# Optimization experiments

Measured on AMD Instinct MI355X. Metric: run time of the kernel, lower is better.

Reference implementation:

```python
import jax, jax.numpy as jnp
import numpy as np
from jax import lax

N_IN = 200000
N_OUT = 400000
K3 = 27
M = 100000
C_IN = 128
C_OUT = 128
EPS = 1e-5


def setup_inputs() -> dict:
    key = jax.random.key(0)
    k1, k2, k3, k4 = jax.random.split(key, 4)
    feats = jax.random.normal(k1, (N_IN, C_IN), dtype=jnp.float32)
    W = jax.random.normal(k2, (K3, C_IN, C_OUT), dtype=jnp.float32) * (1.0 / np.sqrt(C_IN))
    gamma = jnp.ones((C_OUT,), dtype=jnp.float32)
    beta = jnp.zeros((C_OUT,), dtype=jnp.float32)
    in_maps = jax.random.randint(k3, (K3, M), 0, N_IN, dtype=jnp.int32)
    out_maps = jax.random.randint(k4, (K3, M), 0, N_OUT, dtype=jnp.int32)
    return {"feats": feats, "W": W, "gamma": gamma, "beta": beta,
            "in_maps": in_maps, "out_maps": out_maps, "n_out": N_OUT}


def sparse_conv_transpose(feats, W, in_maps, out_maps, n_out):
    # gather-GEMM-scatter over K3 kernel offsets (fixed small set -> scan)
    out0 = jnp.zeros((n_out, W.shape[-1]), dtype=feats.dtype)

    def body(out, xs):
        im, om, Wk = xs                      # [M], [M], [C_in, C_out]
        contrib = feats[im] @ Wk             # gather [M, C_in] -> GEMM -> [M, C_out]
        return out.at[om].add(contrib), None  # scatter-add

    out, _ = lax.scan(body, out0, (in_maps, out_maps, W))
    return out


def reference(feats, W, gamma, beta, in_maps, out_maps, n_out):
    out = sparse_conv_transpose(feats, W, in_maps, out_maps, n_out)  # [N_out, C_out]
    # MinkowskiBatchNorm (training mode): per-channel stats over all points
    mean = jnp.mean(out, axis=0)
    var = jnp.var(out, axis=0)
    y = (out - mean) * lax.rsqrt(var + EPS) * gamma + beta
    return y
```

## Files before the change

kernel.cpp:

```cpp
#include <hip/hip_runtime.h>
#include <hip/hip_fp16.h>

#define K3c    27
#define Mc     100000
#define NINc   200000
#define NOUTc  400000
#define Cc     128
#define EPSc   1e-5f

#define NBUCK  6250
#define NCNTA  (K3c * NBUCK)
#define NCNTG  NOUTc
#define BPK    391
#define SCANBA 165
#define SCANBG 391

#define WS_STATS   0u
#define WS_CNTA    4096u
#define WS_AUXA    679936u
#define WS_CNTG    681984u
#define WS_AUXG    2282496u
#define WS_WFH     2285568u
#define WS_WFL     3170304u
#define WS_SIMA    4055040u
#define WS_PGA     14855040u
#define WS_CBUF    25657344u

typedef __attribute__((ext_vector_type(8))) short short8;
typedef __attribute__((ext_vector_type(4))) float f32x4;

__device__ inline unsigned fbits(float f) { return __builtin_bit_cast(unsigned, f); }
__device__ inline float bfloat(unsigned u) { return __builtin_bit_cast(float, u); }

__device__ inline unsigned pack_hi2(float f0, float f1) {
    return (fbits(f0) >> 16) | (fbits(f1) & 0xFFFF0000u);
}
__device__ inline float trunc_bf16_f(float f) { return bfloat(fbits(f) & 0xFFFF0000u); }

__device__ inline unsigned short bf16_rne(float f) {
    unsigned u = fbits(f);
    u += 0x7FFFu + ((u >> 16) & 1u);
    return (unsigned short)(u >> 16);
}

__device__ inline unsigned short f2h(float f) { return __half_as_ushort(__float2half(f)); }
__device__ inline float h2f(unsigned short u) { return __half2float(__ushort_as_half(u)); }

__device__ inline void storeC(unsigned short* p, float v) { *p = f2h(v); }
__device__ inline void storeC(float* p, float v) { *p = v; }

__global__ __launch_bounds__(256) void zero3_kernel(float* __restrict__ stats,
                                                    unsigned* __restrict__ cntA,
                                                    unsigned* __restrict__ cntG) {
    int idx = blockIdx.x * 256 + threadIdx.x;
    if (idx < NCNTA) cntA[idx] = 0u;
    if (idx < NCNTG) cntG[idx] = 0u;
    if (idx < 512) stats[idx] = 0.f;
}

__global__ __launch_bounds__(256) void wprep_kernel(const float* __restrict__ W,
                                                    short8* __restrict__ wfh,
                                                    short8* __restrict__ wfl) {
    int tid = blockIdx.x * 256 + threadIdx.x;
    int k     = tid >> 11;
    int rem   = tid & 2047;
    int kstep = rem >> 9;
    int cb    = (rem >> 6) & 7;
    int lane  = rem & 63;
    int n   = cb * 16 + (lane & 15);
    int kk0 = kstep * 32 + (lane >> 4) * 8;
    const float* src = W + k * (Cc * Cc) + kk0 * Cc + n;
    short8 h, l;
#pragma unroll
    for (int j = 0; j < 8; ++j) {
        float f = src[j * Cc];
        unsigned short hb = bf16_rne(f);
        h[j] = (short)hb;
        float hf = bfloat(((unsigned)hb) << 16);
        l[j] = (short)bf16_rne(f - hf);
    }
    wfh[tid] = h;
    wfl[tid] = l;
}

__global__ __launch_bounds__(256) void hist3_kernel(const int* __restrict__ out_maps,
                                                    unsigned* __restrict__ cntA,
                                                    unsigned* __restrict__ cntG) {
    int b = blockIdx.x;
    int k = b / BPK;
    int m = (b - k * BPK) * 256 + threadIdx.x;
    if (m < Mc) {
        int om = out_maps[k * Mc + m];
        atomicAdd(&cntA[k * NBUCK + (om >> 6)], 1u);
        atomicAdd(&cntG[om], 1u);
    }
}

__global__ __launch_bounds__(1024) void scan_a(unsigned* __restrict__ c,
                                               unsigned* __restrict__ aux, int n) {
    __shared__ unsigned lds[1024];
    const int t = threadIdx.x;
    const int i = blockIdx.x * 1024 + t;
    unsigned v = (i < n) ? c[i] : 0u;
    lds[t] = v;
    __syncthreads();
    for (int off = 1; off < 1024; off <<= 1) {
        unsigned x = (t >= off) ? lds[t - off] : 0u;
        __syncthreads();
        lds[t] += x;
        __syncthreads();
    }
    if (i < n) c[i] = lds[t] - v;
    if (t == 1023) aux[blockIdx.x] = lds[1023];
}

__global__ __launch_bounds__(1024) void scan_b(unsigned* __restrict__ aux, int nb) {
    __shared__ unsigned lds[1024];
    const int t = threadIdx.x;
    unsigned v = (t < nb) ? aux[t] : 0u;
    lds[t] = v;
    __syncthreads();
    for (int off = 1; off < 1024; off <<= 1) {
        unsigned x = (t >= off) ? lds[t - off] : 0u;
        __syncthreads();
        lds[t] += x;
        __syncthreads();
    }
    if (t < nb) aux[t] = lds[t] - v;
}

__global__ __launch_bounds__(1024) void scan_c(unsigned* __restrict__ c,
                                               const unsigned* __restrict__ aux, int n) {
    const int i = blockIdx.x * 1024 + threadIdx.x;
    if (i < n) c[i] += aux[blockIdx.x];
}

__global__ __launch_bounds__(256) void build3_kernel(const int* __restrict__ in_maps,
                                                     const int* __restrict__ out_maps,
                                                     unsigned* __restrict__ cntA,
                                                     unsigned* __restrict__ cntG,
                                                     int* __restrict__ simA,
                                                     unsigned* __restrict__ pgA) {
    int b = blockIdx.x;
    int k = b / BPK;
    int m = (b - k * BPK) * 256 + threadIdx.x;
    if (m < Mc) {
        int om = out_maps[k * Mc + m];
        int im = in_maps[k * Mc + m];
        unsigned posA = atomicAdd(&cntA[k * NBUCK + (om >> 6)], 1u);
        unsigned posG = atomicAdd(&cntG[om], 1u);
        simA[posA] = im;
        pgA[posA]  = posG;
    }
}

template <typename ST>
__global__ __launch_bounds__(256) void phaseA_kernel(
    const float* __restrict__ feats,
    const short8* __restrict__ wfh, const short8* __restrict__ wfl,
    const unsigned* __restrict__ endA,
    const unsigned* __restrict__ endG,
    const int* __restrict__ simA, const unsigned* __restrict__ pgA,
    ST* __restrict__ cbuf, int B0, int B1, int CPSL, unsigned capRows)
{
    __shared__ short fsh[64 * 136];
    __shared__ short fsl[64 * 136];
    __shared__ unsigned posr[64];

    const int t  = threadIdx.x;
    const int bx = blockIdx.x;
    const int k  = bx / CPSL;
    const int ci = bx - k * CPSL;
    const unsigned lo = (k == 0 && B0 == 0) ? 0u : endA[k * NBUCK + B0 - 1];
    const unsigned hi = endA[k * NBUCK + B1 - 1];
    const unsigned start = lo + (unsigned)ci * 64u;
    if (start >= hi) return;
    const int valid = (int)(hi - start < 64u ? hi - start : 64u);
    const unsigned slabBase = (B0 == 0) ? 0u : endG[B0 * 64 - 1];

    {
        const int r  = t >> 2;
        const int cg = t & 3;
        const bool ok = (r < valid);
        long im = ok ? (long)simA[start + r] : 0;
        if (cg == 0) posr[r] = ok ? (pgA[start + r] - slabBase) : 0xFFFFFFFFu;
        const float4* src4 = (const float4*)(feats + im * Cc + cg * 32);
        unsigned* fh32 = (unsigned*)fsh;
        unsigned* fl32 = (unsigned*)fsl;
#pragma unroll
        for (int j = 0; j < 8; ++j) {
            float4 v = ok ? src4[j] : make_float4(0.f, 0.f, 0.f, 0.f);
            int col = cg * 32 + j * 4;
            int idx = r * 68 + (col >> 1);
            fh32[idx]     = pack_hi2(v.x, v.y);
            fh32[idx + 1] = pack_hi2(v.z, v.w);
            float lx = v.x - trunc_bf16_f(v.x);
            float ly = v.y - trunc_bf16_f(v.y);
            float lz = v.z - trunc_bf16_f(v.z);
            float lw = v.w - trunc_bf16_f(v.w);
            fl32[idx]     = pack_hi2(lx, ly);
            fl32[idx + 1] = pack_hi2(lz, lw);
        }
    }
    __syncthreads();

    const int wave = t >> 6;
    const int lane = t & 63;
    const int m    = lane & 15;
    const int quad = lane >> 4;

    f32x4 acc[8];
#pragma unroll
    for (int cb = 0; cb < 8; ++cb) acc[cb] = (f32x4){0.f, 0.f, 0.f, 0.f};

    const int arow = wave * 16 + m;
    for (int kstep = 0; kstep < 4; ++kstep) {
        const short* ah = fsh + arow * 136 + kstep * 32 + quad * 8;
        const short* al = fsl + arow * 136 + kstep * 32 + quad * 8;
        short8 a_hi = *(const short8*)ah;
        short8 a_lo = *(const short8*)al;
        int fb = ((k * 4 + kstep) * 8) * 64 + lane;
#pragma unroll
        for (int cb = 0; cb < 8; ++cb) {
            short8 b_hi = wfh[fb + cb * 64];
            short8 b_lo = wfl[fb + cb * 64];
            acc[cb] = __builtin_amdgcn_mfma_f32_16x16x32_bf16(a_hi, b_hi, acc[cb], 0, 0, 0);
            acc[cb] = __builtin_amdgcn_mfma_f32_16x16x32_bf16(a_lo, b_hi, acc[cb], 0, 0, 0);
            acc[cb] = __builtin_amdgcn_mfma_f32_16x16x32_bf16(a_hi, b_lo, acc[cb], 0, 0, 0);
        }
    }

    const int rbase = wave * 16 + quad * 4;
#pragma unroll
    for (int reg = 0; reg < 4; ++reg) {
        int row = rbase + reg;
        if (row < valid) {
            unsigned rp = posr[row];
            if (rp < capRows) {
                ST* dst = cbuf + (size_t)rp * Cc + m;
#pragma unroll
                for (int cb = 0; cb < 8; ++cb)
                    storeC(dst + cb * 16, acc[cb][reg]);
            }
        }
    }
}

template <typename ST>
__global__ __launch_bounds__(256) void phaseB_kernel(
    const ST* __restrict__ cbuf, const unsigned* __restrict__ endG,
    float* __restrict__ out, int B0)
{
    __shared__ unsigned ends[66];
    const int t = threadIdx.x;
    const int bucket = B0 + blockIdx.x;
    const int om0 = bucket * 64;
    if (t < 65) ends[t] = (om0 + t == 0) ? 0u : endG[om0 + t - 1];
    if (t == 65) ends[65] = (B0 == 0) ? 0u : endG[B0 * 64 - 1];
    __syncthreads();
    const unsigned sbase = ends[65];
    const int r  = t >> 2;
    const int cg = t & 3;
    unsigned e0 = ends[r] - sbase;
    unsigned e1 = ends[r + 1] - sbase;

    float a[32];
#pragma unroll
    for (int j = 0; j < 32; ++j) a[j] = 0.f;

    for (unsigned e = e0; e < e1; ++e) {
        const ST* src = cbuf + (size_t)e * Cc + cg * 32;
        if constexpr (sizeof(ST) == 2) {
            const short8* s8 = (const short8*)src;
#pragma unroll
            for (int p = 0; p < 4; ++p) {
                short8 v = s8[p];
#pragma unroll
                for (int j = 0; j < 8; ++j)
                    a[p * 8 + j] += h2f((unsigned short)v[j]);
            }
        } else {
            const float4* f4 = (const float4*)src;
#pragma unroll
            for (int p = 0; p < 8; ++p) {
                float4 v = f4[p];
                a[p * 4 + 0] += v.x; a[p * 4 + 1] += v.y;
                a[p * 4 + 2] += v.z; a[p * 4 + 3] += v.w;
            }
        }
    }

    float4* dst = (float4*)(out + (size_t)(om0 + r) * Cc + cg * 32);
#pragma unroll
    for (int p = 0; p < 8; ++p)
        dst[p] = make_float4(a[p * 4], a[p * 4 + 1], a[p * 4 + 2], a[p * 4 + 3]);
}

__global__ __launch_bounds__(256) void stats_kernel(const float4* __restrict__ out4,
                                                    float* __restrict__ stats) {
    const int t  = threadIdx.x;
    const int tx = t & 31;
    const int ty = t >> 5;

    float4 s = make_float4(0.f, 0.f, 0.f, 0.f);
    float4 q = make_float4(0.f, 0.f, 0.f, 0.f);
    int row0 = blockIdx.x * 400 + ty;
    for (int j = 0; j < 50; ++j) {
        float4 v = out4[(row0 + j * 8) * 32 + tx];
        s.x += v.x; s.y += v.y; s.z += v.z; s.w += v.w;
        q.x += v.x * v.x; q.y += v.y * v.y; q.z += v.z * v.z; q.w += v.w * v.w;
    }

    __shared__ float4 redS[256];
    __shared__ float4 redQ[256];
    redS[t] = s; redQ[t] = q;
    __syncthreads();
    if (ty == 0) {
#pragma unroll
        for (int jj = 1; jj < 8; ++jj) {
            float4 o = redS[jj * 32 + tx];
            s.x += o.x; s.y += o.y; s.z += o.z; s.w += o.w;
            float4 oq = redQ[jj * 32 + tx];
            q.x += oq.x; q.y += oq.y; q.z += oq.z; q.w += oq.w;
        }
        unsafeAtomicAdd(&stats[tx * 4 + 0], s.x);
        unsafeAtomicAdd(&stats[tx * 4 + 1], s.y);
        unsafeAtomicAdd(&stats[tx * 4 + 2], s.z);
        unsafeAtomicAdd(&stats[tx * 4 + 3], s.w);
        unsafeAtomicAdd(&stats[Cc + tx * 4 + 0], q.x);
        unsafeAtomicAdd(&stats[Cc + tx * 4 + 1], q.y);
        unsafeAtomicAdd(&stats[Cc + tx * 4 + 2], q.z);
        unsafeAtomicAdd(&stats[Cc + tx * 4 + 3], q.w);
    }
}

__global__ void finalize_kernel(const float* __restrict__ gamma,
                                const float* __restrict__ beta,
                                float* __restrict__ stats) {
    int c = threadIdx.x;
    float inv_n = 1.0f / (float)NOUTc;
    float mean = stats[c] * inv_n;
    float var  = stats[Cc + c] * inv_n - mean * mean;
    float scale = gamma[c] * rsqrtf(var + EPSc);
    stats[2 * Cc + c] = scale;
    stats[3 * Cc + c] = beta[c] - mean * scale;
}

__global__ __launch_bounds__(256) void norm_kernel(float4* __restrict__ out4,
                                                   const float* __restrict__ stats) {
    const float4* stats4 = (const float4*)stats;
    int idx0 = blockIdx.x * blockDim.x + threadIdx.x;
    int c4 = idx0 & 31;
    float4 sc = stats4[64 + c4];
    float4 sh = stats4[96 + c4];
    const int n4 = NOUTc * (Cc / 4);
    const int stride = gridDim.x * blockDim.x;
    for (int i = idx0; i < n4; i += stride) {
        float4 v = out4[i];
        v.x = v.x * sc.x + sh.x;
        v.y = v.y * sc.y + sh.y;
        v.z = v.z * sc.z + sh.z;
        v.w = v.w * sc.w + sh.w;
        out4[i] = v;
    }
}

extern "C" void kernel_launch(void* const* d_in, const int* in_sizes, int n_in,
                              void* d_out, int out_size, void* d_ws, size_t ws_size,
                              hipStream_t stream) {
    const float* feats    = (const float*)d_in[0];
    const float* W        = (const float*)d_in[1];
    const float* gamma    = (const float*)d_in[2];
    const float* beta     = (const float*)d_in[3];
    const int*   in_maps  = (const int*)d_in[4];
    const int*   out_maps = (const int*)d_in[5];
    float* out = (float*)d_out;

    char* ws = (char*)d_ws;
    float*    stats = (float*)(ws + WS_STATS);
    unsigned* cntA  = (unsigned*)(ws + WS_CNTA);
    unsigned* auxA  = (unsigned*)(ws + WS_AUXA);
    unsigned* cntG  = (unsigned*)(ws + WS_CNTG);
    unsigned* auxG  = (unsigned*)(ws + WS_AUXG);
    short8*   wfh   = (short8*)(ws + WS_WFH);
    short8*   wfl   = (short8*)(ws + WS_WFL);
    int*      simA  = (int*)(ws + WS_SIMA);
    unsigned* pgA   = (unsigned*)(ws + WS_PGA);

    zero3_kernel<<<1563, 256, 0, stream>>>(stats, cntA, cntG);
    wprep_kernel<<<216, 256, 0, stream>>>(W, wfh, wfl);
    hist3_kernel<<<K3c * BPK, 256, 0, stream>>>(out_maps, cntA, cntG);
    scan_a<<<SCANBA, 1024, 0, stream>>>(cntA, auxA, NCNTA);
    scan_b<<<1, 1024, 0, stream>>>(auxA, SCANBA);
    scan_c<<<SCANBA, 1024, 0, stream>>>(cntA, auxA, NCNTA);
    scan_a<<<SCANBG, 1024, 0, stream>>>(cntG, auxG, NCNTG);
    scan_b<<<1, 1024, 0, stream>>>(auxG, SCANBG);
    scan_c<<<SCANBG, 1024, 0, stream>>>(cntG, auxG, NCNTG);
    build3_kernel<<<K3c * BPK, 256, 0, stream>>>(in_maps, out_maps, cntA, cntG,
                                                 simA, pgA);

    size_t cap = (ws_size > WS_CBUF) ? (size_t)(ws_size - WS_CBUF) : 0;
    auto slabs_for = [&](size_t eb) -> int {
        for (int n = 1; n <= 64; ++n) {
            double rows = 2700000.0 / n * 1.04 + 4096.0;
            if ((size_t)rows * 128ull * eb <= cap) return n;
        }
        return -1;
    };
    int n32 = slabs_for(4);
    int n16 = slabs_for(2);
    bool use_f32 = (n32 > 0 && n32 <= 8);
    int nslab = use_f32 ? n32 : (n16 > 0 ? n16 : 64);
    const int SB = (NBUCK + nslab - 1) / nslab;
    const int CPSL = (int)(16.0 * SB * 1.10 / 64.0) + 3;

    for (int s = 0; s < nslab; ++s) {
        int B0 = s * SB;
        int B1 = (B0 + SB < NBUCK) ? B0 + SB : NBUCK;
        if (B0 >= B1) break;
        if (use_f32) {
            unsigned capRows = (unsigned)(cap / (128ull * 4ull));
            float* cbuf = (float*)(ws + WS_CBUF);
            phaseA_kernel<float><<<K3c * CPSL, 256, 0, stream>>>(
                feats, wfh, wfl, cntA, cntG, simA, pgA, cbuf, B0, B1, CPSL, capRows);
            phaseB_kernel<float><<<B1 - B0, 256, 0, stream>>>(cbuf, cntG, out, B0);
        } else {
            unsigned capRows = (unsigned)(cap / (128ull * 2ull));
            unsigned short* cbuf = (unsigned short*)(ws + WS_CBUF);
            phaseA_kernel<unsigned short><<<K3c * CPSL, 256, 0, stream>>>(
                feats, wfh, wfl, cntA, cntG, simA, pgA, cbuf, B0, B1, CPSL, capRows);
            phaseB_kernel<unsigned short><<<B1 - B0, 256, 0, stream>>>(cbuf, cntG, out, B0);
        }
    }

    stats_kernel<<<1000, 256, 0, stream>>>((const float4*)out, stats);
    finalize_kernel<<<1, 128, 0, stream>>>(gamma, beta, stats);
    norm_kernel<<<4096, 256, 0, stream>>>((float4*)out, stats);
}
```

Baseline: 2.515 ms.

## Process four 64-row chunks per phaseA block with register-resident weights and prefetch

Each phaseA block now handles up to four 64-row chunks instead of one. Each wave keeps its slice of the weight matrix (two output column blocks, hi and lo) in registers for the whole block instead of reloading it from global memory per chunk. The gather of the next chunk's feature rows is issued before the MFMA work on the current chunk, and launch bounds request 3 blocks per CU. The aim is to cut weight reloads and hide gather latency, at the cost of higher register pressure and fewer, longer blocks.

```diff
diff --git a/kernel.cpp b/kernel.cpp
--- a/kernel.cpp
+++ b/kernel.cpp
@@ -14,6 +14,7 @@
 #define BPK    391
 #define SCANBA 165
 #define SCANBG 391
+#define NCH    4
 
 #define WS_STATS   0u
 #define WS_CNTA    4096u
@@ -155,94 +156,140 @@
 }
 
 template <typename ST>
-__global__ __launch_bounds__(256) void phaseA_kernel(
+__global__ __launch_bounds__(256, 3) void phaseA_kernel(
     const float* __restrict__ feats,
     const short8* __restrict__ wfh, const short8* __restrict__ wfl,
     const unsigned* __restrict__ endA,
     const unsigned* __restrict__ endG,
     const int* __restrict__ simA, const unsigned* __restrict__ pgA,
-    ST* __restrict__ cbuf, int B0, int B1, int CPSL, unsigned capRows)
+    ST* __restrict__ cbuf, int B0, int B1, int BPSL, unsigned capRows)
 {
     __shared__ short fsh[64 * 136];
     __shared__ short fsl[64 * 136];
-    __shared__ unsigned posr[64];
+    __shared__ int      ims[NCH * 64];
+    __shared__ unsigned poss[NCH * 64];
 
     const int t  = threadIdx.x;
     const int bx = blockIdx.x;
-    const int k  = bx / CPSL;
-    const int ci = bx - k * CPSL;
+    const int k  = bx / BPSL;
+    const int bi = bx - k * BPSL;
     const unsigned lo = (k == 0 && B0 == 0) ? 0u : endA[k * NBUCK + B0 - 1];
     const unsigned hi = endA[k * NBUCK + B1 - 1];
-    const unsigned start = lo + (unsigned)ci * 64u;
-    if (start >= hi) return;
-    const int valid = (int)(hi - start < 64u ? hi - start : 64u);
+    const unsigned start0 = lo + (unsigned)bi * (NCH * 64u);
+    if (start0 >= hi) return;
+    const unsigned avail = hi - start0;
+    const int navail = (int)(avail < (unsigned)(NCH * 64) ? avail : (unsigned)(NCH * 64));
+    const int nchunk = (navail + 63) >> 6;
     const unsigned slabBase = (B0 == 0) ? 0u : endG[B0 * 64 - 1];
 
-    {
-        const int r  = t >> 2;
-        const int cg = t & 3;
-        const bool ok = (r < valid);
-        long im = ok ? (long)simA[start + r] : 0;
-        if (cg == 0) posr[r] = ok ? (pgA[start + r] - slabBase) : 0xFFFFFFFFu;
-        const float4* src4 = (const float4*)(feats + im * Cc + cg * 32);
-        unsigned* fh32 = (unsigned*)fsh;
-        unsigned* fl32 = (unsigned*)fsl;
-#pragma unroll
-        for (int j = 0; j < 8; ++j) {
-            float4 v = ok ? src4[j] : make_float4(0.f, 0.f, 0.f, 0.f);
-            int col = cg * 32 + j * 4;
-            int idx = r * 68 + (col >> 1);
-            fh32[idx]     = pack_hi2(v.x, v.y);
-            fh32[idx + 1] = pack_hi2(v.z, v.w);
-            float lx = v.x - trunc_bf16_f(v.x);
-            float ly = v.y - trunc_bf16_f(v.y);
-            float lz = v.z - trunc_bf16_f(v.z);
-            float lw = v.w - trunc_bf16_f(v.w);
-            fl32[idx]     = pack_hi2(lx, ly);
-            fl32[idx + 1] = pack_hi2(lz, lw);
-        }
-    }
-    __syncthreads();
+    if (t < navail) {
+        ims[t]  = simA[start0 + t];
+        poss[t] = pgA[start0 + t] - slabBase;
+    } else {
+        ims[t]  = 0;
+        poss[t] = 0xFFFFFFFFu;
+    }
 
     const int wave = t >> 6;
     const int lane = t & 63;
     const int m    = lane & 15;
     const int quad = lane >> 4;
-
-    f32x4 acc[8];
-#pragma unroll
-    for (int cb = 0; cb < 8; ++cb) acc[cb] = (f32x4){0.f, 0.f, 0.f, 0.f};
-
-    const int arow = wave * 16 + m;
-    for (int kstep = 0; kstep < 4; ++kstep) {
-        const short* ah = fsh + arow * 136 + kstep * 32 + quad * 8;
-        const short* al = fsl + arow * 136 + kstep * 32 + quad * 8;
-        short8 a_hi = *(const short8*)ah;
-        short8 a_lo = *(const short8*)al;
-        int fb = ((k * 4 + kstep) * 8) * 64 + lane;
-#pragma unroll
-        for (int cb = 0; cb < 8; ++cb) {
-            short8 b_hi = wfh[fb + cb * 64];
-            short8 b_lo = wfl[fb + cb * 64];
-            acc[cb] = __builtin_amdgcn_mfma_f32_16x16x32_bf16(a_hi, b_hi, acc[cb], 0, 0, 0);
-            acc[cb] = __builtin_amdgcn_mfma_f32_16x16x32_bf16(a_lo, b_hi, acc[cb], 0, 0, 0);
-            acc[cb] = __builtin_amdgcn_mfma_f32_16x16x32_bf16(a_hi, b_lo, acc[cb], 0, 0, 0);
-        }
-    }
-
-    const int rbase = wave * 16 + quad * 4;
-#pragma unroll
-    for (int reg = 0; reg < 4; ++reg) {
-        int row = rbase + reg;
-        if (row < valid) {
-            unsigned rp = posr[row];
-            if (rp < capRows) {
-                ST* dst = cbuf + (size_t)rp * Cc + m;
-#pragma unroll
-                for (int cb = 0; cb < 8; ++cb)
-                    storeC(dst + cb * 16, acc[cb][reg]);
+    const int r    = t >> 2;
+    const int cg   = t & 3;
+
+    short8 Bh[8], Bl[8];
+#pragma unroll
+    for (int ks = 0; ks < 4; ++ks) {
+        const int fb = ((k * 4 + ks) * 8) * 64 + lane;
+#pragma unroll
+        for (int cbi = 0; cbi < 2; ++cbi) {
+            Bh[ks * 2 + cbi] = wfh[fb + (wave * 2 + cbi) * 64];
+            Bl[ks * 2 + cbi] = wfl[fb + (wave * 2 + cbi) * 64];
+        }
+    }
+
+    __syncthreads();
+
+    float4 fr[8];
+    {
+        const float4* s4 = (const float4*)(feats + (long)ims[r] * Cc + cg * 32);
+#pragma unroll
+        for (int j = 0; j < 8; ++j) fr[j] = s4[j];
+    }
+
+    for (int c = 0; c < nchunk; ++c) {
+        {
+            unsigned* fh32 = (unsigned*)fsh;
+            unsigned* fl32 = (unsigned*)fsl;
+#pragma unroll
+            for (int j = 0; j < 8; ++j) {
+                float4 v = fr[j];
+                int idx = r * 68 + cg * 16 + j * 2;
+                uint2 hh, ll;
+                hh.x = pack_hi2(v.x, v.y);
+                hh.y = pack_hi2(v.z, v.w);
+                float lx = v.x - trunc_bf16_f(v.x);
+                float ly = v.y - trunc_bf16_f(v.y);
+                float lz = v.z - trunc_bf16_f(v.z);
+                float lw = v.w - trunc_bf16_f(v.w);
+                ll.x = pack_hi2(lx, ly);
+                ll.y = pack_hi2(lz, lw);
+                *(uint2*)(fh32 + idx) = hh;
+                *(uint2*)(fl32 + idx) = ll;
             }
         }
+        if (c + 1 < nchunk) {
+            const float4* s4 =
+                (const float4*)(feats + (long)ims[(c + 1) * 64 + r] * Cc + cg * 32);
+#pragma unroll
+            for (int j = 0; j < 8; ++j) fr[j] = s4[j];
+        }
+        __syncthreads();
+
+        f32x4 acc[4][2];
+#pragma unroll
+        for (int sub = 0; sub < 4; ++sub) {
+            acc[sub][0] = (f32x4){0.f, 0.f, 0.f, 0.f};
+            acc[sub][1] = (f32x4){0.f, 0.f, 0.f, 0.f};
+        }
+
+#pragma unroll
+        for (int sub = 0; sub < 4; ++sub) {
+            const short* ah = fsh + (sub * 16 + m) * 136 + quad * 8;
+            const short* al = fsl + (sub * 16 + m) * 136 + quad * 8;
+#pragma unroll
+            for (int ks = 0; ks < 4; ++ks) {
+                short8 a_hi = *(const short8*)(ah + ks * 32);
+                short8 a_lo = *(const short8*)(al + ks * 32);
+#pragma unroll
+                for (int cbi = 0; cbi < 2; ++cbi) {
+                    acc[sub][cbi] = __builtin_amdgcn_mfma_f32_16x16x32_bf16(
+                        a_hi, Bh[ks * 2 + cbi], acc[sub][cbi], 0, 0, 0);
+                    acc[sub][cbi] = __builtin_amdgcn_mfma_f32_16x16x32_bf16(
+                        a_lo, Bh[ks * 2 + cbi], acc[sub][cbi], 0, 0, 0);
+                    acc[sub][cbi] = __builtin_amdgcn_mfma_f32_16x16x32_bf16(
+                        a_hi, Bl[ks * 2 + cbi], acc[sub][cbi], 0, 0, 0);
+                }
+            }
+        }
+
+        const int cvalid = (navail - c * 64) < 64 ? (navail - c * 64) : 64;
+#pragma unroll
+        for (int sub = 0; sub < 4; ++sub) {
+#pragma unroll
+            for (int reg = 0; reg < 4; ++reg) {
+                int row = sub * 16 + quad * 4 + reg;
+                if (row < cvalid) {
+                    unsigned rp = poss[c * 64 + row];
+                    if (rp < capRows) {
+                        ST* dst = cbuf + (size_t)rp * Cc + m;
+                        storeC(dst + (wave * 2 + 0) * 16, acc[sub][0][reg]);
+                        storeC(dst + (wave * 2 + 1) * 16, acc[sub][1][reg]);
+                    }
+                }
+            }
+        }
+        __syncthreads();
     }
 }
 
@@ -413,6 +460,7 @@
     int nslab = use_f32 ? n32 : (n16 > 0 ? n16 : 64);
     const int SB = (NBUCK + nslab - 1) / nslab;
     const int CPSL = (int)(16.0 * SB * 1.10 / 64.0) + 3;
+    const int BPSL = (CPSL + NCH - 1) / NCH;
 
     for (int s = 0; s < nslab; ++s) {
         int B0 = s * SB;
@@ -421,14 +469,14 @@
         if (use_f32) {
             unsigned capRows = (unsigned)(cap / (128ull * 4ull));
             float* cbuf = (float*)(ws + WS_CBUF);
-            phaseA_kernel<float><<<K3c * CPSL, 256, 0, stream>>>(
-                feats, wfh, wfl, cntA, cntG, simA, pgA, cbuf, B0, B1, CPSL, capRows);
+            phaseA_kernel<float><<<K3c * BPSL, 256, 0, stream>>>(
+                feats, wfh, wfl, cntA, cntG, simA, pgA, cbuf, B0, B1, BPSL, capRows);
             phaseB_kernel<float><<<B1 - B0, 256, 0, stream>>>(cbuf, cntG, out, B0);
         } else {
             unsigned capRows = (unsigned)(cap / (128ull * 2ull));
             unsigned short* cbuf = (unsigned short*)(ws + WS_CBUF);
-            phaseA_kernel<unsigned short><<<K3c * CPSL, 256, 0, stream>>>(
-                feats, wfh, wfl, cntA, cntG, simA, pgA, cbuf, B0, B1, CPSL, capRows);
+            phaseA_kernel<unsigned short><<<K3c * BPSL, 256, 0, stream>>>(
+                feats, wfh, wfl, cntA, cntG, simA, pgA, cbuf, B0, B1, BPSL, capRows);
             phaseB_kernel<unsigned short><<<B1 - B0, 256, 0, stream>>>(cbuf, cntG, out, B0);
         }
     }
```

Result: faster. 2.014 ms (-19.9%).
